# Optimization experiments

Measured on AMD Instinct MI355X. Metric: run time of the kernel, lower is better.

## Reference

```python
import jax, jax.numpy as jnp
import numpy as np

HEADS = 32
KV_HEADS = 8
HEAD_DIM = 128
ROPE_THETA = 10000.0


def _rope_tables(position_ids, head_dim, dtype):
    # position_ids: [S] int
    inv_freq = 1.0 / (ROPE_THETA ** (jnp.arange(0, head_dim, 2, dtype=jnp.float32) / head_dim))
    freqs = position_ids.astype(jnp.float32)[:, None] * inv_freq[None, :]   # [S, hd/2]
    emb = jnp.concatenate([freqs, freqs], axis=-1)                          # [S, hd]
    return jnp.cos(emb).astype(dtype), jnp.sin(emb).astype(dtype)


def _rotate_half(x):
    h = x.shape[-1] // 2
    return jnp.concatenate([-x[..., h:], x[..., :h]], axis=-1)


def setup_inputs() -> dict:
    key = jax.random.key(0)
    ks = jax.random.split(key, 5)
    B, S, D = 2, 2048, 4096
    kv_dim = KV_HEADS * HEAD_DIM
    s = 0.02
    return {
        "hidden_states": jax.random.normal(ks[0], (B, S, D), jnp.float32),
        "position_ids": jnp.arange(S, dtype=jnp.int64 if jax.config.jax_enable_x64 else jnp.int32),
        "wq": jax.random.normal(ks[1], (D, D), jnp.float32) * s,
        "wk": jax.random.normal(ks[2], (kv_dim, D), jnp.float32) * s,
        "wv": jax.random.normal(ks[3], (kv_dim, D), jnp.float32) * s,
        "wo": jax.random.normal(ks[4], (D, D), jnp.float32) * s,
    }


def reference(hidden_states, position_ids, wq, wk, wv, wo):
    B, S, D = hidden_states.shape
    groups = HEADS // KV_HEADS

    # Q/K/V projections (nn.Linear: x @ W.T), split into heads -> [B, H, S, hd]
    q = (hidden_states @ wq.T).reshape(B, S, HEADS, HEAD_DIM).transpose(0, 2, 1, 3)
    k = (hidden_states @ wk.T).reshape(B, S, KV_HEADS, HEAD_DIM).transpose(0, 2, 1, 3)
    v = (hidden_states @ wv.T).reshape(B, S, KV_HEADS, HEAD_DIM).transpose(0, 2, 1, 3)

    # RoPE
    cos, sin = _rope_tables(position_ids, HEAD_DIM, q.dtype)  # [S, hd]
    q = q * cos + _rotate_half(q) * sin
    k = k * cos + _rotate_half(k) * sin

    # GQA: expand KV heads to match Q heads
    k = jnp.repeat(k, groups, axis=1)  # [B, H, S, hd]
    v = jnp.repeat(v, groups, axis=1)

    # causal SDPA
    scale = 1.0 / jnp.sqrt(jnp.asarray(HEAD_DIM, q.dtype))
    scores = jnp.einsum("bhqd,bhkd->bhqk", q, k) * scale
    causal = jnp.tril(jnp.ones((S, S), dtype=bool))
    scores = jnp.where(causal, scores, jnp.finfo(scores.dtype).min)
    probs = jax.nn.softmax(scores, axis=-1)
    attn = jnp.einsum("bhqk,bhkd->bhqd", probs, v)  # [B, H, S, hd]

    # merge heads + output projection
    attn = attn.transpose(0, 2, 1, 3).reshape(B, S, D)
    return attn @ wo.T
```

## Files before the change

kernel.cpp:

```cpp
#include <hip/hip_runtime.h>
#include <hip/hip_bf16.h>
#include <math.h>

typedef __attribute__((ext_vector_type(8))) short short8;
typedef __attribute__((ext_vector_type(4))) float f32x4;
typedef __attribute__((ext_vector_type(16))) float f32x16;
typedef __attribute__((ext_vector_type(4))) unsigned int u32x4;
typedef __attribute__((ext_vector_type(2))) int i32x2;

#define BATCH   2
#define SLEN    2048
#define DMODEL  4096
#define NHEADS  32
#define KVHEADS 8
#define HD      128
#define KVDIM   (KVHEADS*HD)
#define MROWS   (BATCH*SLEN)
#define NQKV    (DMODEL + 2*KVDIM)

#define GLDS16(gp, lp) __builtin_amdgcn_global_load_lds( \
    (const __attribute__((address_space(1))) void*)(gp), \
    (__attribute__((address_space(3))) void*)(lp), 16, 0, 0)

static __device__ __forceinline__ unsigned short bf16bits(float x) {
    __hip_bfloat16 h = __float2bfloat16(x);
    return *(unsigned short*)&h;
}
static __device__ __forceinline__ float bf2f(unsigned short u) {
    __hip_bfloat16 h = *(__hip_bfloat16*)&u;
    return __bfloat162float(h);
}
static __device__ __forceinline__ unsigned cvtpk(float a, float b) {
    unsigned r;
    asm("v_cvt_pk_bf16_f32 %0, %1, %2" : "=v"(r) : "v"(a), "v"(b));
    return r;
}

__global__ __launch_bounds__(256) void cast_k(const float* __restrict__ in,
                                              unsigned short* __restrict__ out, long n) {
    long i = ((long)blockIdx.x * 256 + threadIdx.x) * 4;
    if (i >= n) return;
    float4 v = *(const float4*)(in + i);
    union { unsigned short h[4]; uint2 u; } c;
    c.h[0] = bf16bits(v.x); c.h[1] = bf16bits(v.y);
    c.h[2] = bf16bits(v.z); c.h[3] = bf16bits(v.w);
    *(uint2*)(out + i) = c.u;
}

__global__ void rope_table_k(const int* __restrict__ pos,
                             float* __restrict__ cosT, float* __restrict__ sinT) {
    int s = blockIdx.x;
    int d = threadIdx.x;
    float p = (float)pos[s];
    float inv = powf(10000.0f, -(float)(2 * d) / 128.0f);
    float ang = p * inv;
    cosT[s * 64 + d] = cosf(ang);
    sinT[s * 64 + d] = sinf(ang);
}

__global__ void rope_bf_k(unsigned short* __restrict__ x,
                          const float* __restrict__ cosT, const float* __restrict__ sinT,
                          int nh, int ld, float mul) {
    int idx = blockIdx.x * 256 + threadIdx.x;
    int d = idx & 63;
    int rest = idx >> 6;
    int h = rest % nh;
    int row = rest / nh;
    int s = row & (SLEN - 1);
    float c  = cosT[s * 64 + d] * mul;
    float sn = sinT[s * 64 + d] * mul;
    unsigned short* base = x + (size_t)row * ld + h * HD;
    float x1 = bf2f(base[d]), x2 = bf2f(base[d + 64]);
    base[d]      = bf16bits(x1 * c - x2 * sn);
    base[d + 64] = bf16bits(x2 * c + x1 * sn);
}

__global__ __launch_bounds__(256) void vtrans_k(const unsigned short* __restrict__ V, int ldv,
                                                unsigned short* __restrict__ Vt) {
    __shared__ unsigned short L[64][144];
    const int t = threadIdx.x;
    const int s0 = blockIdx.x * 64;
    const int bk = blockIdx.y;
    const int b = bk >> 3, kvh = bk & 7;
    #pragma unroll
    for (int j = 0; j < 4; ++j) {
        int idx = t + j * 256;
        int row = idx >> 4;
        int c8  = (idx & 15) * 8;
        *(short8*)&L[row][c8] =
            *(const short8*)(V + ((size_t)b * SLEN + s0 + row) * ldv + kvh * HD + c8);
    }
    __syncthreads();
    {
        int d  = t >> 1;
        int sh = (t & 1) * 32;
        unsigned short tmp[32];
        #pragma unroll
        for (int j = 0; j < 32; ++j) tmp[j] = L[sh + j][d];
        unsigned short* dst = Vt + ((size_t)bk * HD + d) * SLEN + s0 + sh;
        #pragma unroll
        for (int j = 0; j < 4; ++j)
            *(short8*)(dst + j * 8) = *(const short8*)(tmp + j * 8);
    }
}

template<typename CT>
__global__ __launch_bounds__(512, 2) void gemm256(
    const unsigned short* __restrict__ A, int lda,
    const unsigned short* __restrict__ W, int ldw,
    CT* __restrict__ C, int ldc,
    int M, int N, int K)
{
    __shared__ unsigned short Asl[2][2][128 * 64];
    __shared__ unsigned short Bsl[2][2][128 * 64];

    const int t = threadIdx.x;
    const int w = t >> 6, lane = t & 63;
    const int m0 = blockIdx.y * 256, n0 = blockIdx.x * 256;
    const int wm = (w >> 2) * 128;
    const int wn = (w & 3) * 64;
    const int fr = lane & 15, hi = lane >> 4;

    f32x4 acc[8][4];
    #pragma unroll
    for (int i = 0; i < 8; ++i)
        #pragma unroll
        for (int j = 0; j < 4; ++j)
            acc[i][j] = (f32x4){0.f, 0.f, 0.f, 0.f};

    const int sr = t >> 3;
    const int sl = t & 7;

    auto STAGE = [&](int buf, int kt) {
        const int k0 = kt * 64;
        #pragma unroll
        for (int half = 0; half < 2; ++half) {
            #pragma unroll
            for (int j = 0; j < 2; ++j) {
                int row  = j * 64 + sr;
                int scol = k0 + ((sl ^ (row & 7)) << 3);
                GLDS16(A + (size_t)(m0 + half * 128 + row) * lda + scol,
                       &Asl[buf][half][j * 4096 + w * 512]);
                GLDS16(W + (size_t)(n0 + half * 128 + row) * ldw + scol,
                       &Bsl[buf][half][j * 4096 + w * 512]);
            }
        }
    };

    STAGE(0, 0);
    const int NT = K >> 6;
    int buf = 0;
    for (int kt = 0; kt < NT; ++kt) {
        if (kt + 1 < NT) {
            STAGE(buf ^ 1, kt + 1);
            asm volatile("s_waitcnt vmcnt(8)" ::: "memory");
        } else {
            asm volatile("s_waitcnt vmcnt(0)" ::: "memory");
        }
        __builtin_amdgcn_s_barrier();
        __builtin_amdgcn_sched_barrier(0);

        const unsigned short* Ah = Asl[buf][w >> 2];
        const unsigned short* Bh = Bsl[buf][wn >> 7];

        short8 bfr[4][2];
        #pragma unroll
        for (int j = 0; j < 4; ++j) {
            int lr = (wn & 127) + j * 16 + fr;
            int swz = lr & 7;
            #pragma unroll
            for (int kk = 0; kk < 2; ++kk) {
                int s0 = kk * 4 + hi;
                bfr[j][kk] = *(const short8*)&Bh[lr * 64 + ((s0 ^ swz) << 3)];
            }
        }
        #pragma unroll
        for (int i = 0; i < 8; ++i) {
            int lr = i * 16 + fr;
            int swz = lr & 7;
            short8 a0 = *(const short8*)&Ah[lr * 64 + (((0 + hi) ^ swz) << 3)];
            short8 a1 = *(const short8*)&Ah[lr * 64 + (((4 + hi) ^ swz) << 3)];
            __builtin_amdgcn_s_setprio(1);
            #pragma unroll
            for (int j = 0; j < 4; ++j) {
                acc[i][j] = __builtin_amdgcn_mfma_f32_16x16x32_bf16(a0, bfr[j][0], acc[i][j], 0, 0, 0);
                acc[i][j] = __builtin_amdgcn_mfma_f32_16x16x32_bf16(a1, bfr[j][1], acc[i][j], 0, 0, 0);
            }
            __builtin_amdgcn_s_setprio(0);
        }

        __builtin_amdgcn_sched_barrier(0);
        __builtin_amdgcn_s_barrier();
        buf ^= 1;
    }

    const int crow = (lane >> 4) * 4, ccol = lane & 15;
    #pragma unroll
    for (int i = 0; i < 8; ++i)
        #pragma unroll
        for (int j = 0; j < 4; ++j) {
            CT* cp = C + (size_t)(m0 + wm + i * 16 + crow) * ldc + (n0 + wn + j * 16 + ccol);
            #pragma unroll
            for (int r = 0; r < 4; ++r) {
                if constexpr (sizeof(CT) == 2)
                    cp[(size_t)r * ldc] = bf16bits(acc[i][j][r]);
                else
                    cp[(size_t)r * ldc] = acc[i][j][r];
            }
        }
}

__global__ __launch_bounds__(256, 2) void flash_mfma32(
    const unsigned short* __restrict__ Qb, int ldq,
    const unsigned short* __restrict__ Kb, int ldk,
    const unsigned short* __restrict__ Vt,
    unsigned short* __restrict__ Ob)
{
    __shared__ unsigned short Ks[2][64 * 128];
    __shared__ unsigned short Vs[2][128 * 64];

    const int t = threadIdx.x;
    const int wid = t >> 6, lane = t & 63;
    const int qt = (int)gridDim.x - 1 - (int)blockIdx.x;
    const int bh = blockIdx.y;
    const int b = bh >> 5, h = bh & 31, kvh = h >> 2;
    const int lq = lane & 31;
    const int hl = lane >> 5;
    const int qw0 = qt * 128 + wid * 32;
    const int qg = qw0 + lq;
    const size_t qrowg = (size_t)b * SLEN + qg;

    const unsigned short* Kg0 = Kb + (size_t)b * SLEN * ldk + kvh * HD;
    const unsigned short* Vg0 = Vt + (size_t)(b * KVHEADS + kvh) * HD * SLEN;

    auto STAGE = [&](int buf, int kt) {
        const unsigned short* Kg = Kg0 + (size_t)kt * 64 * ldk;
        #pragma unroll
        for (int i = 0; i < 4; ++i) {
            int row = i * 16 + (t >> 4);
            int colel = ((((t & 15) << 4) ^ ((row & 15) << 4)) >> 1);
            GLDS16(Kg + (size_t)row * ldk + colel, &Ks[buf][i * 2048 + wid * 512]);
        }
        const unsigned short* Vg = Vg0 + kt * 64;
        #pragma unroll
        for (int i = 0; i < 4; ++i) {
            int row = i * 32 + (t >> 3);
            int colel = ((((t & 7) << 4) ^ ((row & 7) << 4)) >> 1);
            GLDS16(Vg + (size_t)row * SLEN + colel, &Vs[buf][i * 2048 + wid * 512]);
        }
    };

    STAGE(0, 0);
    short8 qf[8];
    {
        const unsigned short* qp = Qb + qrowg * ldq + h * HD + hl * 8;
        #pragma unroll
        for (int dt = 0; dt < 8; ++dt)
            qf[dt] = *(const short8*)(qp + dt * 16);
    }

    f32x16 accO[4];
    #pragma unroll
    for (int db = 0; db < 4; ++db)
        #pragma unroll
        for (int r = 0; r < 16; ++r) accO[db][r] = 0.f;
    float m_i = -INFINITY, l_i = 0.f;

    const int ntmax = 2 * qt + 2;
    int p = 0;
    for (int kt = 0; kt < ntmax; ++kt) {
        if (kt + 1 < ntmax) {
            STAGE(p ^ 1, kt + 1);
            asm volatile("s_waitcnt vmcnt(8)" ::: "memory");
        } else {
            asm volatile("s_waitcnt vmcnt(0)" ::: "memory");
        }
        __builtin_amdgcn_s_barrier();
        __builtin_amdgcn_sched_barrier(0);

        const unsigned short* Kp = Ks[p];
        const unsigned short* Vp = Vs[p];

        f32x16 sc[2];
        #pragma unroll
        for (int blk = 0; blk < 2; ++blk) {
            #pragma unroll
            for (int r = 0; r < 16; ++r) sc[blk][r] = 0.f;
            __builtin_amdgcn_s_setprio(1);
            #pragma unroll
            for (int dt = 0; dt < 8; ++dt) {
                int krow = blk * 32 + lq;
                int kb = krow * 256 + ((dt * 32 + hl * 16) ^ ((krow & 15) << 4));
                short8 kf = *(const short8*)(Kp + (kb >> 1));
                sc[blk] = __builtin_amdgcn_mfma_f32_32x32x16_bf16(kf, qf[dt], sc[blk], 0, 0, 0);
            }
            __builtin_amdgcn_s_setprio(0);
        }

        if (kt * 64 + 63 > qw0) {
            #pragma unroll
            for (int blk = 0; blk < 2; ++blk)
                #pragma unroll
                for (int r = 0; r < 16; ++r) {
                    int kv = kt * 64 + blk * 32 + (r & 3) + 8 * (r >> 2) + 4 * hl;
                    if (kv > qg) sc[blk][r] = -INFINITY;
                }
        }

        float pmax = sc[0][0];
        #pragma unroll
        for (int r = 1; r < 16; ++r) pmax = fmaxf(pmax, sc[0][r]);
        #pragma unroll
        for (int r = 0; r < 16; ++r) pmax = fmaxf(pmax, sc[1][r]);
        {
            i32x2 mr = __builtin_amdgcn_permlane32_swap(__float_as_int(pmax), __float_as_int(pmax), false, false);
            pmax = fmaxf(__int_as_float(mr.x), __int_as_float(mr.y));
        }

        if (!__all(pmax <= m_i + 8.0f)) {
            float mn = fmaxf(m_i, pmax);
            float al = exp2f(m_i - mn);
            m_i = mn;
            l_i *= al;
            #pragma unroll
            for (int db = 0; db < 4; ++db)
                #pragma unroll
                for (int r = 0; r < 16; ++r) accO[db][r] *= al;
        }

        float rs = 0.f;
        #pragma unroll
        for (int blk = 0; blk < 2; ++blk)
            #pragma unroll
            for (int r = 0; r < 16; ++r) {
                float pv = exp2f(sc[blk][r] - m_i);
                sc[blk][r] = pv;
                rs += pv;
            }
        {
            i32x2 sr = __builtin_amdgcn_permlane32_swap(__float_as_int(rs), __float_as_int(rs), false, false);
            rs = __int_as_float(sr.x) + __int_as_float(sr.y);
        }
        l_i += rs;

        short8 pf[4];
        #pragma unroll
        for (int blk = 0; blk < 2; ++blk) {
            unsigned c01 = cvtpk(sc[blk][0],  sc[blk][1]);
            unsigned c23 = cvtpk(sc[blk][2],  sc[blk][3]);
            unsigned c45 = cvtpk(sc[blk][4],  sc[blk][5]);
            unsigned c67 = cvtpk(sc[blk][6],  sc[blk][7]);
            i32x2 sA = __builtin_amdgcn_permlane32_swap((int)c01, (int)c45, false, false);
            i32x2 sB = __builtin_amdgcn_permlane32_swap((int)c23, (int)c67, false, false);
            u32x4 f0 = {(unsigned)sA.x, (unsigned)sB.x, (unsigned)sA.y, (unsigned)sB.y};
            pf[blk * 2] = *(short8*)&f0;
            unsigned c89 = cvtpk(sc[blk][8],  sc[blk][9]);
            unsigned cab = cvtpk(sc[blk][10], sc[blk][11]);
            unsigned ccd = cvtpk(sc[blk][12], sc[blk][13]);
            unsigned cef = cvtpk(sc[blk][14], sc[blk][15]);
            i32x2 sC = __builtin_amdgcn_permlane32_swap((int)c89, (int)ccd, false, false);
            i32x2 sD = __builtin_amdgcn_permlane32_swap((int)cab, (int)cef, false, false);
            u32x4 f1 = {(unsigned)sC.x, (unsigned)sD.x, (unsigned)sC.y, (unsigned)sD.y};
            pf[blk * 2 + 1] = *(short8*)&f1;
        }

        #pragma unroll
        for (int db = 0; db < 4; ++db) {
            __builtin_amdgcn_s_setprio(1);
            #pragma unroll
            for (int ks = 0; ks < 4; ++ks) {
                int vrow = db * 32 + lq;
                int vb = vrow * 128 + ((ks * 32 + hl * 16) ^ ((vrow & 7) << 4));
                short8 vf = *(const short8*)(Vp + (vb >> 1));
                accO[db] = __builtin_amdgcn_mfma_f32_32x32x16_bf16(vf, pf[ks], accO[db], 0, 0, 0);
            }
            __builtin_amdgcn_s_setprio(0);
        }

        __builtin_amdgcn_sched_barrier(0);
        __builtin_amdgcn_s_barrier();
        p ^= 1;
    }

    float inv = 1.0f / l_i;
    unsigned short* orow = Ob + qrowg * DMODEL + h * HD;
    #pragma unroll
    for (int db = 0; db < 4; ++db)
        #pragma unroll
        for (int rq = 0; rq < 4; ++rq) {
            unsigned w0 = cvtpk(accO[db][rq * 4 + 0] * inv, accO[db][rq * 4 + 1] * inv);
            unsigned w1 = cvtpk(accO[db][rq * 4 + 2] * inv, accO[db][rq * 4 + 3] * inv);
            uint2 pkd; pkd.x = w0; pkd.y = w1;
            *(uint2*)(orow + db * 32 + rq * 8 + hl * 4) = pkd;
        }
}

extern "C" void kernel_launch(void* const* d_in, const int* in_sizes, int n_in,
                              void* d_out, int out_size, void* d_ws, size_t ws_size,
                              hipStream_t stream) {
    const float* hs  = (const float*)d_in[0];
    const int*   pos = (const int*)d_in[1];
    const float* wq  = (const float*)d_in[2];
    const float* wk  = (const float*)d_in[3];
    const float* wv  = (const float*)d_in[4];
    const float* wo  = (const float*)d_in[5];
    float* out = (float*)d_out;

    char* ws = (char*)d_ws;
    unsigned short* hs_bf   = (unsigned short*)(ws);
    unsigned short* wqkv_bf = (unsigned short*)(ws + ((size_t)32  << 20));
    unsigned short* wo_bf   = (unsigned short*)(ws + ((size_t)80  << 20));
    unsigned short* qkv_bf  = (unsigned short*)(ws + ((size_t)112 << 20));
    unsigned short* Vtb     = (unsigned short*)(ws + ((size_t)160 << 20));
    unsigned short* Obf     = (unsigned short*)(ws + ((size_t)168 << 20));
    float*          cosT    = (float*)(ws + ((size_t)200 << 20));
    float*          sinT    = (float*)(ws + ((size_t)200 << 20) + (size_t)SLEN * 64 * 4);

    const long nHS = (long)MROWS * DMODEL;
    const long nWQ = (long)DMODEL * DMODEL;
    const long nWK = (long)KVDIM * DMODEL;

    rope_table_k<<<SLEN, 64, 0, stream>>>(pos, cosT, sinT);

    cast_k<<<nHS / 4 / 256, 256, 0, stream>>>(hs, hs_bf, nHS);
    cast_k<<<nWQ / 4 / 256, 256, 0, stream>>>(wq, wqkv_bf, nWQ);
    cast_k<<<nWK / 4 / 256, 256, 0, stream>>>(wk, wqkv_bf + (size_t)DMODEL * DMODEL, nWK);
    cast_k<<<nWK / 4 / 256, 256, 0, stream>>>(wv, wqkv_bf + (size_t)(DMODEL + KVDIM) * DMODEL, nWK);
    cast_k<<<nWQ / 4 / 256, 256, 0, stream>>>(wo, wo_bf, nWQ);

    gemm256<unsigned short><<<dim3(NQKV/256, MROWS/256), 512, 0, stream>>>(
        hs_bf, DMODEL, wqkv_bf, DMODEL, qkv_bf, NQKV, MROWS, NQKV, DMODEL);

    const float qmul = 0.088388347648318447f * 1.4426950408889634f;
    rope_bf_k<<<(MROWS * NHEADS  * 64) / 256, 256, 0, stream>>>(qkv_bf,          cosT, sinT, NHEADS,  NQKV, qmul);
    rope_bf_k<<<(MROWS * KVHEADS * 64) / 256, 256, 0, stream>>>(qkv_bf + DMODEL, cosT, sinT, KVHEADS, NQKV, 1.0f);
    vtrans_k<<<dim3(SLEN/64, BATCH*KVHEADS), 256, 0, stream>>>(qkv_bf + DMODEL + KVDIM, NQKV, Vtb);

    flash_mfma32<<<dim3(SLEN/128, BATCH*NHEADS), 256, 0, stream>>>(
        qkv_bf, NQKV, qkv_bf + DMODEL, NQKV, Vtb, Obf);

    gemm256<float><<<dim3(DMODEL/256, MROWS/256), 512, 0, stream>>>(
        Obf, DMODEL, wo_bf, DMODEL, out, DMODEL, MROWS, DMODEL, DMODEL);
}
```

Measured before the change: 687.8 us.

## Interleave prefetch with MFMA quarters, swizzle workgroup order, relax launch bounds

The GEMM main loop is split into four quarters. Each quarter issues one slice of the next tile's global-to-LDS loads, then runs its MFMAs, with fine-grained vmcnt waits and barriers replacing the single wait at the top of each iteration. Workgroup IDs are remapped with a stride-8 swizzle to improve L2 reuse of A and W tiles. Launch bounds drop to one block per CU, which frees registers but lowers occupancy. The extra barriers add synchronisation overhead, and the swizzle assumes the workgroup count is divisible by 8.

```diff
diff --git a/kernel.cpp b/kernel.cpp
--- a/kernel.cpp
+++ b/kernel.cpp
@@ -105,7 +105,7 @@
 }
 
 template<typename CT>
-__global__ __launch_bounds__(512, 2) void gemm256(
+__global__ __launch_bounds__(512, 1) void gemm256(
     const unsigned short* __restrict__ A, int lda,
     const unsigned short* __restrict__ W, int ldw,
     CT* __restrict__ C, int ldc,
@@ -116,7 +116,13 @@
 
     const int t = threadIdx.x;
     const int w = t >> 6, lane = t & 63;
-    const int m0 = blockIdx.y * 256, n0 = blockIdx.x * 256;
+
+    const int gx = gridDim.x;
+    const int nwg = gx * gridDim.y;
+    const int orig = blockIdx.y * gx + blockIdx.x;
+    const int swzid = (orig & 7) * (nwg >> 3) + (orig >> 3);
+    const int m0 = (swzid / gx) * 256, n0 = (swzid % gx) * 256;
+
     const int wm = (w >> 2) * 128;
     const int wn = (w & 3) * 64;
     const int fr = lane & 15, hi = lane >> 4;
@@ -130,67 +136,97 @@
 
     const int sr = t >> 3;
     const int sl = t & 7;
-
-    auto STAGE = [&](int buf, int kt) {
-        const int k0 = kt * 64;
-        #pragma unroll
-        for (int half = 0; half < 2; ++half) {
+    const int wv512 = w * 512;
+
+    {
+        #pragma unroll
+        for (int hh = 0; hh < 4; ++hh) {
             #pragma unroll
             for (int j = 0; j < 2; ++j) {
-                int row  = j * 64 + sr;
-                int scol = k0 + ((sl ^ (row & 7)) << 3);
-                GLDS16(A + (size_t)(m0 + half * 128 + row) * lda + scol,
-                       &Asl[buf][half][j * 4096 + w * 512]);
-                GLDS16(W + (size_t)(n0 + half * 128 + row) * ldw + scol,
-                       &Bsl[buf][half][j * 4096 + w * 512]);
-            }
-        }
-    };
-
-    STAGE(0, 0);
+                const int row = j * 64 + sr;
+                const int scol = (sl ^ (row & 7)) << 3;
+                if (hh < 2)
+                    GLDS16(W + (size_t)(n0 + hh * 128 + row) * ldw + scol,
+                           &Bsl[0][hh][j * 4096 + wv512]);
+                else
+                    GLDS16(A + (size_t)(m0 + (hh - 2) * 128 + row) * lda + scol,
+                           &Asl[0][hh - 2][j * 4096 + wv512]);
+            }
+        }
+        asm volatile("s_waitcnt vmcnt(2)" ::: "memory");
+        __builtin_amdgcn_s_barrier();
+        __builtin_amdgcn_sched_barrier(0);
+    }
+
     const int NT = K >> 6;
     int buf = 0;
     for (int kt = 0; kt < NT; ++kt) {
-        if (kt + 1 < NT) {
-            STAGE(buf ^ 1, kt + 1);
-            asm volatile("s_waitcnt vmcnt(8)" ::: "memory");
-        } else {
-            asm volatile("s_waitcnt vmcnt(0)" ::: "memory");
-        }
-        __builtin_amdgcn_s_barrier();
-        __builtin_amdgcn_sched_barrier(0);
-
         const unsigned short* Ah = Asl[buf][w >> 2];
-        const unsigned short* Bh = Bsl[buf][wn >> 7];
-
+        const unsigned short* Bh = Bsl[buf][(w & 3) >> 1];
+        const bool pf = (kt + 1 < NT);
+        const int k0n = (kt + 1) << 6;
         short8 bfr[4][2];
-        #pragma unroll
-        for (int j = 0; j < 4; ++j) {
-            int lr = (wn & 127) + j * 16 + fr;
-            int swz = lr & 7;
-            #pragma unroll
-            for (int kk = 0; kk < 2; ++kk) {
-                int s0 = kk * 4 + hi;
-                bfr[j][kk] = *(const short8*)&Bh[lr * 64 + ((s0 ^ swz) << 3)];
-            }
-        }
-        #pragma unroll
-        for (int i = 0; i < 8; ++i) {
-            int lr = i * 16 + fr;
-            int swz = lr & 7;
-            short8 a0 = *(const short8*)&Ah[lr * 64 + (((0 + hi) ^ swz) << 3)];
-            short8 a1 = *(const short8*)&Ah[lr * 64 + (((4 + hi) ^ swz) << 3)];
+
+        #pragma unroll
+        for (int q = 0; q < 4; ++q) {
+            if (q == 0) {
+                #pragma unroll
+                for (int j = 0; j < 4; ++j) {
+                    const int lr = (wn & 127) + j * 16 + fr;
+                    const int sz = lr & 7;
+                    bfr[j][0] = *(const short8*)&Bh[lr * 64 + (((0 + hi) ^ sz) << 3)];
+                    bfr[j][1] = *(const short8*)&Bh[lr * 64 + (((4 + hi) ^ sz) << 3)];
+                }
+            }
+            short8 af[2][2];
+            #pragma unroll
+            for (int ii = 0; ii < 2; ++ii) {
+                const int lr = q * 32 + ii * 16 + fr;
+                const int sz = lr & 7;
+                af[ii][0] = *(const short8*)&Ah[lr * 64 + (((0 + hi) ^ sz) << 3)];
+                af[ii][1] = *(const short8*)&Ah[lr * 64 + (((4 + hi) ^ sz) << 3)];
+            }
+
+            if (pf) {
+                #pragma unroll
+                for (int j = 0; j < 2; ++j) {
+                    const int row = j * 64 + sr;
+                    const int scol = k0n + ((sl ^ (row & 7)) << 3);
+                    if (q < 2)
+                        GLDS16(W + (size_t)(n0 + q * 128 + row) * ldw + scol,
+                               &Bsl[buf ^ 1][q][j * 4096 + wv512]);
+                    else
+                        GLDS16(A + (size_t)(m0 + (q - 2) * 128 + row) * lda + scol,
+                               &Asl[buf ^ 1][q - 2][j * 4096 + wv512]);
+                }
+            }
+
+            __builtin_amdgcn_sched_barrier(0);
+            __builtin_amdgcn_s_barrier();
+            __builtin_amdgcn_sched_barrier(0);
+
             __builtin_amdgcn_s_setprio(1);
             #pragma unroll
-            for (int j = 0; j < 4; ++j) {
-                acc[i][j] = __builtin_amdgcn_mfma_f32_16x16x32_bf16(a0, bfr[j][0], acc[i][j], 0, 0, 0);
-                acc[i][j] = __builtin_amdgcn_mfma_f32_16x16x32_bf16(a1, bfr[j][1], acc[i][j], 0, 0, 0);
-            }
+            for (int ii = 0; ii < 2; ++ii)
+                #pragma unroll
+                for (int j = 0; j < 4; ++j) {
+                    acc[q * 2 + ii][j] = __builtin_amdgcn_mfma_f32_16x16x32_bf16(
+                        af[ii][0], bfr[j][0], acc[q * 2 + ii][j], 0, 0, 0);
+                    acc[q * 2 + ii][j] = __builtin_amdgcn_mfma_f32_16x16x32_bf16(
+                        af[ii][1], bfr[j][1], acc[q * 2 + ii][j], 0, 0, 0);
+                }
             __builtin_amdgcn_s_setprio(0);
-        }
-
-        __builtin_amdgcn_sched_barrier(0);
-        __builtin_amdgcn_s_barrier();
+
+            if (q == 1) {
+                if (pf) asm volatile("s_waitcnt vmcnt(4)" ::: "memory");
+                else    asm volatile("s_waitcnt vmcnt(0)" ::: "memory");
+            } else if (q == 3 && pf) {
+                asm volatile("s_waitcnt vmcnt(2)" ::: "memory");
+            }
+            __builtin_amdgcn_sched_barrier(0);
+            __builtin_amdgcn_s_barrier();
+            __builtin_amdgcn_sched_barrier(0);
+        }
         buf ^= 1;
     }
 
```

Result: faster. 635.6 us (-7.6%).
